# Kernel tuning notes

Measured on AMD Instinct MI355X. Metric: run time of the kernel, lower is better.

## Reference

```python
import jax, jax.numpy as jnp
import numpy as np

EPS = 1e-20

def setup_inputs() -> dict:
    key = jax.random.key(0)
    k1, k2, k3, k4 = jax.random.split(key, 4)
    B, C, H, W, K = 8, 64, 512, 512, 16
    hex_list = ["0x1a1c2c", "0x5d275d", "0xb13e53", "0xef7d57", "0xffcd75", "0xa7f070",
                "0x38b764", "0x257179", "0x29366f", "0x3b5dc9", "0x41a6f6", "0x73eff7",
                "0xf4f4f4", "0x94b0c2", "0x566c86", "0x333c57"]
    rgb = np.array([[int(h[2:][i:i+2], 16) for i in (0, 2, 4)] for h in hex_list],
                   dtype=np.float32) / 255.0
    return {
        "x": jax.random.normal(k1, (B, C, H, W), dtype=jnp.float32),
        "conv_w": jax.random.normal(k2, (K, C), dtype=jnp.float32) * (1.0 / np.sqrt(C)),
        "conv_b": jax.random.normal(k3, (K,), dtype=jnp.float32) * 0.01,
        "palette": jnp.asarray(rgb),                      # [K, 3], fixed constant
        "unif": jax.random.uniform(k4, (B, H, W, K), dtype=jnp.float32),
    }

def reference(x, conv_w, conv_b, palette, unif):
    # 1x1 conv == per-pixel matmul over channel dim: [B,C,H,W] x [K,C] -> [B,K,H,W]
    logits = jnp.einsum('bchw,kc->bkhw', x, conv_w) + conv_b[None, :, None, None]
    color_prob = jax.nn.softmax(logits, axis=1)           # [B,K,H,W]
    # weighted sum over palette: sum_k prob[b,k,h,w] * palette[k,c]
    blended = jnp.einsum('bkhw,kc->bchw', color_prob, palette)  # [B,3,H,W]
    # multinomial sample via Gumbel-max over K (same distribution as torch.multinomial)
    logp = jax.nn.log_softmax(logits, axis=1).transpose(0, 2, 3, 1)  # [B,H,W,K]
    gumbel = -jnp.log(-jnp.log(unif + EPS) + EPS)
    idx = jnp.argmax(logp + gumbel, axis=-1)              # [B,H,W] int
    discrete = palette[idx].transpose(0, 3, 1, 2)         # [B,3,H,W]
    # straight-through estimator
    pixel_art = jax.lax.stop_gradient(discrete - blended) + blended
    return pixel_art
```

## Files before the change

### kernel.cpp

```cpp
#include <hip/hip_runtime.h>
#include <math.h>

#define HW_ (512 * 512)
#define C_ 64
#define K_ 16
#define B_ 8

__global__ __launch_bounds__(256) void transpose_w_kernel(const float* __restrict__ w,
                                                          float* __restrict__ wt) {
    int i = blockIdx.x * blockDim.x + threadIdx.x;
    if (i < K_ * C_) {
        int k = i >> 6;
        int c = i & 63;
        wt[c * K_ + k] = w[i];
    }
}

__global__ __launch_bounds__(256) void quantizer_kernel(
    const float* __restrict__ x,
    const float* __restrict__ wt,
    const float* __restrict__ bias,
    const float* __restrict__ palette,
    const float* __restrict__ unif,
    float* __restrict__ out)
{
    const int total = B_ * HW_;
    int tid = blockIdx.x * blockDim.x + threadIdx.x;
    int stride = gridDim.x * blockDim.x;

    for (int p = tid; p < total; p += stride) {
        int b = p >> 18;
        int hw = p & (HW_ - 1);
        const float* xp = x + ((size_t)b * C_) * (size_t)HW_ + (size_t)hw;

        float acc[K_];
        #pragma unroll
        for (int k = 0; k < K_; ++k) acc[k] = bias[k];

        for (int c = 0; c < C_; c += 4) {
            float x0 = xp[(size_t)(c + 0) * HW_];
            float x1 = xp[(size_t)(c + 1) * HW_];
            float x2 = xp[(size_t)(c + 2) * HW_];
            float x3 = xp[(size_t)(c + 3) * HW_];
            const float* wp = wt + c * K_;
            #pragma unroll
            for (int k = 0; k < K_; ++k) {
                float a = acc[k];
                a = fmaf(x0, wp[k],          a);
                a = fmaf(x1, wp[K_ + k],     a);
                a = fmaf(x2, wp[2 * K_ + k], a);
                a = fmaf(x3, wp[3 * K_ + k], a);
                acc[k] = a;
            }
        }

        float m = acc[0];
        #pragma unroll
        for (int k = 1; k < K_; ++k) m = fmaxf(m, acc[k]);
        float s = 0.0f;
        #pragma unroll
        for (int k = 0; k < K_; ++k) s += expf(acc[k] - m);
        float ls = logf(s);

        const float4* up4 = reinterpret_cast<const float4*>(unif + (size_t)p * K_);
        float u[K_];
        #pragma unroll
        for (int q = 0; q < 4; ++q) {
            float4 v = up4[q];
            u[q * 4 + 0] = v.x; u[q * 4 + 1] = v.y;
            u[q * 4 + 2] = v.z; u[q * 4 + 3] = v.w;
        }
        float best = -INFINITY;
        int bi = 0;
        #pragma unroll
        for (int k = 0; k < K_; ++k) {
            float g = -logf(-logf(u[k] + 1e-20f) + 1e-20f);
            float t = (acc[k] - m) - ls + g;
            if (t > best) { best = t; bi = k; }
        }

        float pr = palette[bi * 3 + 0];
        float pg = palette[bi * 3 + 1];
        float pb = palette[bi * 3 + 2];
        size_t obase = (size_t)b * 3 * HW_ + (size_t)hw;
        out[obase]                    = pr;
        out[obase + (size_t)HW_]      = pg;
        out[obase + 2 * (size_t)HW_]  = pb;
    }
}

extern "C" void kernel_launch(void* const* d_in, const int* in_sizes, int n_in,
                              void* d_out, int out_size, void* d_ws, size_t ws_size,
                              hipStream_t stream) {
    const float* x       = (const float*)d_in[0];
    const float* conv_w  = (const float*)d_in[1];
    const float* conv_b  = (const float*)d_in[2];
    const float* palette = (const float*)d_in[3];
    const float* unif    = (const float*)d_in[4];
    float* out = (float*)d_out;
    float* wt  = (float*)d_ws;

    hipLaunchKernelGGL(transpose_w_kernel, dim3(4), dim3(256), 0, stream, conv_w, wt);

    const int blocks = 2048;
    hipLaunchKernelGGL(quantizer_kernel, dim3(blocks), dim3(256), 0, stream,
                       x, wt, conv_b, palette, unif, out);
}
```

Before: 160.9 us.

## Process four pixels per thread with float4 loads and stores

Each thread now handles four adjacent pixels in place of looping over a grid-stride range. Channel inputs are read as float4 and results written as float4, and each weight load is shared across four pixels' accumulators. Per-pixel softmax and Gumbel argmax run per lane. This cuts load/store instruction count and weight reloads for a bandwidth-bound kernel, at the cost of a 64-float accumulator tile raising register pressure; a min-blocks hint is added to the launch bounds.

```diff
diff --git a/kernel.cpp b/kernel.cpp
--- a/kernel.cpp
+++ b/kernel.cpp
@@ -16,7 +16,7 @@
     }
 }
 
-__global__ __launch_bounds__(256) void quantizer_kernel(
+__global__ __launch_bounds__(256, 4) void quantizer_kernel(
     const float* __restrict__ x,
     const float* __restrict__ wt,
     const float* __restrict__ bias,
@@ -24,69 +24,73 @@
     const float* __restrict__ unif,
     float* __restrict__ out)
 {
-    const int total = B_ * HW_;
-    int tid = blockIdx.x * blockDim.x + threadIdx.x;
-    int stride = gridDim.x * blockDim.x;
+    int t = blockIdx.x * blockDim.x + threadIdx.x;
+    int p0 = t << 2;
+    int b = p0 >> 18;
+    int hw = p0 & (HW_ - 1);
+    const float* xp = x + (size_t)b * C_ * HW_ + (size_t)hw;
 
-    for (int p = tid; p < total; p += stride) {
-        int b = p >> 18;
-        int hw = p & (HW_ - 1);
-        const float* xp = x + ((size_t)b * C_) * (size_t)HW_ + (size_t)hw;
+    float acc[K_][4];
+    #pragma unroll
+    for (int k = 0; k < K_; ++k) {
+        float bk = bias[k];
+        acc[k][0] = bk; acc[k][1] = bk; acc[k][2] = bk; acc[k][3] = bk;
+    }
 
-        float acc[K_];
+    #pragma unroll 8
+    for (int c = 0; c < C_; ++c) {
+        float4 xv = *reinterpret_cast<const float4*>(xp + (size_t)c * HW_);
+        const float* wp = wt + c * K_;
         #pragma unroll
-        for (int k = 0; k < K_; ++k) acc[k] = bias[k];
+        for (int k = 0; k < K_; ++k) {
+            float w = wp[k];
+            acc[k][0] = fmaf(xv.x, w, acc[k][0]);
+            acc[k][1] = fmaf(xv.y, w, acc[k][1]);
+            acc[k][2] = fmaf(xv.z, w, acc[k][2]);
+            acc[k][3] = fmaf(xv.w, w, acc[k][3]);
+        }
+    }
 
-        for (int c = 0; c < C_; c += 4) {
-            float x0 = xp[(size_t)(c + 0) * HW_];
-            float x1 = xp[(size_t)(c + 1) * HW_];
-            float x2 = xp[(size_t)(c + 2) * HW_];
-            float x3 = xp[(size_t)(c + 3) * HW_];
-            const float* wp = wt + c * K_;
-            #pragma unroll
-            for (int k = 0; k < K_; ++k) {
-                float a = acc[k];
-                a = fmaf(x0, wp[k],          a);
-                a = fmaf(x1, wp[K_ + k],     a);
-                a = fmaf(x2, wp[2 * K_ + k], a);
-                a = fmaf(x3, wp[3 * K_ + k], a);
-                acc[k] = a;
-            }
-        }
-
-        float m = acc[0];
+    float cr[4], cg[4], cb[4];
+    #pragma unroll
+    for (int j = 0; j < 4; ++j) {
+        float m = acc[0][j];
         #pragma unroll
-        for (int k = 1; k < K_; ++k) m = fmaxf(m, acc[k]);
+        for (int k = 1; k < K_; ++k) m = fmaxf(m, acc[k][j]);
         float s = 0.0f;
         #pragma unroll
-        for (int k = 0; k < K_; ++k) s += expf(acc[k] - m);
+        for (int k = 0; k < K_; ++k) s += expf(acc[k][j] - m);
         float ls = logf(s);
 
-        const float4* up4 = reinterpret_cast<const float4*>(unif + (size_t)p * K_);
-        float u[K_];
+        const float4* up4 = reinterpret_cast<const float4*>(unif + ((size_t)p0 + j) * K_);
+        float best = -INFINITY;
+        int bi = 0;
         #pragma unroll
         for (int q = 0; q < 4; ++q) {
             float4 v = up4[q];
-            u[q * 4 + 0] = v.x; u[q * 4 + 1] = v.y;
-            u[q * 4 + 2] = v.z; u[q * 4 + 3] = v.w;
+            float uu0 = v.x, uu1 = v.y, uu2 = v.z, uu3 = v.w;
+            float g0 = -logf(-logf(uu0 + 1e-20f) + 1e-20f);
+            float g1 = -logf(-logf(uu1 + 1e-20f) + 1e-20f);
+            float g2 = -logf(-logf(uu2 + 1e-20f) + 1e-20f);
+            float g3 = -logf(-logf(uu3 + 1e-20f) + 1e-20f);
+            float t0 = (acc[q * 4 + 0][j] - m) - ls + g0;
+            float t1 = (acc[q * 4 + 1][j] - m) - ls + g1;
+            float t2 = (acc[q * 4 + 2][j] - m) - ls + g2;
+            float t3 = (acc[q * 4 + 3][j] - m) - ls + g3;
+            if (t0 > best) { best = t0; bi = q * 4 + 0; }
+            if (t1 > best) { best = t1; bi = q * 4 + 1; }
+            if (t2 > best) { best = t2; bi = q * 4 + 2; }
+            if (t3 > best) { best = t3; bi = q * 4 + 3; }
         }
-        float best = -INFINITY;
-        int bi = 0;
-        #pragma unroll
-        for (int k = 0; k < K_; ++k) {
-            float g = -logf(-logf(u[k] + 1e-20f) + 1e-20f);
-            float t = (acc[k] - m) - ls + g;
-            if (t > best) { best = t; bi = k; }
-        }
+        cr[j] = palette[bi * 3 + 0];
+        cg[j] = palette[bi * 3 + 1];
+        cb[j] = palette[bi * 3 + 2];
+    }
 
-        float pr = palette[bi * 3 + 0];
-        float pg = palette[bi * 3 + 1];
-        float pb = palette[bi * 3 + 2];
-        size_t obase = (size_t)b * 3 * HW_ + (size_t)hw;
-        out[obase]                    = pr;
-        out[obase + (size_t)HW_]      = pg;
-        out[obase + 2 * (size_t)HW_]  = pb;
-    }
+    size_t obase = (size_t)b * 3 * HW_ + (size_t)hw;
+    *reinterpret_cast<float4*>(out + obase)               = make_float4(cr[0], cr[1], cr[2], cr[3]);
+    *reinterpret_cast<float4*>(out + obase + HW_)         = make_float4(cg[0], cg[1], cg[2], cg[3]);
+    *reinterpret_cast<float4*>(out + obase + 2 * HW_)     = make_float4(cb[0], cb[1], cb[2], cb[3]);
 }
 
 extern "C" void kernel_launch(void* const* d_in, const int* in_sizes, int n_in,
@@ -102,7 +106,6 @@
 
     hipLaunchKernelGGL(transpose_w_kernel, dim3(4), dim3(256), 0, stream, conv_w, wt);
 
-    const int blocks = 2048;
-    hipLaunchKernelGGL(quantizer_kernel, dim3(blocks), dim3(256), 0, stream,
+    hipLaunchKernelGGL(quantizer_kernel, dim3(2048), dim3(256), 0, stream,
                        x, wt, conv_b, palette, unif, out);
 }
```

Result: slower. 205.0 us (+27.4%).
